# Performance work log

Hardware: AMD Instinct MI355X
Metric: run time of the kernel (lower is better)

Reference implementation:

```python
import jax, jax.numpy as jnp
import numpy as np

B, T, H, A = 64, 512, 1024, 256  # T == max_sen_len by construction of attention_u
PAD_VAL = -2.0 ** 22


def setup_inputs() -> dict:
    key = jax.random.key(0)
    k1, k2, k3, k4 = jax.random.split(key, 4)
    inputs = jax.random.normal(k1, (B, T, H), dtype=jnp.float32)
    sen_len = jax.random.randint(k2, (B,), 1, T + 1, dtype=jnp.int32)
    W = jax.random.normal(k3, (H, A), dtype=jnp.float32) * (1.0 / np.sqrt(H))
    b = jnp.zeros((A,), dtype=jnp.float32)
    U = jax.random.normal(k4, (A, T), dtype=jnp.float32) * (1.0 / np.sqrt(A))
    return {"inputs": inputs, "sen_len": sen_len, "W": W, "b": b, "U": U}


def reference(inputs, sen_len, W, b, U):
    # Dense with tanh: [B,T,H] @ [H,A] -> [B,T,A]
    alpha = jnp.tanh(jnp.einsum('bth,ha->bta', inputs, W) + b)
    # Score against attention_u: [B,T,A] @ [A,T] -> [B,T,T]
    scores = jnp.einsum('bta,as->bts', alpha, U)
    # sequence mask over last (key) dim, broadcast over query dim
    mask = jnp.arange(T)[None, :] < sen_len[:, None]        # [B,T]
    scores = jnp.where(mask[:, None, :], scores, jnp.float32(PAD_VAL))
    p = jax.nn.softmax(scores, axis=-1)                     # [B,T,T]
    # Weighted sum pooling: [B,T,T] @ [B,T,H] -> [B,T,H]
    Z = jnp.einsum('bts,bsh->bth', p, inputs)
    # dropout: is_training=False -> identity
    return Z
```

## Files before the change

### kernel.cpp

```cpp
#include <hip/hip_runtime.h>
#include <hip/hip_bf16.h>

typedef short short8 __attribute__((ext_vector_type(8)));
typedef short short4v __attribute__((ext_vector_type(4)));
typedef float f32x4 __attribute__((ext_vector_type(4)));
typedef __bf16 bf16x8 __attribute__((ext_vector_type(8)));


template <int ROWS>
__device__ __forceinline__ void stage2(const __hip_bfloat16* __restrict__ g,
                                       int ld, short* lds, int t) {
    const int w = t >> 6;
    const int lane = t & 63;
#pragma unroll
    for (int i = 0; i < ROWS / 64; ++i) {
        const int cb = i * 512 + w * 64;
        const int c = cb + lane;
        const int row = c >> 3;
        const int kc = (c & 7) ^ (row & 7);
        __builtin_amdgcn_global_load_lds((const void*)(g + (long)row * ld + kc * 8),
                                         (void*)(lds + cb * 8), 16, 0, 0);
    }
}

template <int BMt, int BNt, int WR, int WC, int ACT_TANH, int STORE_BF16>
__global__ __launch_bounds__(512, 2) void gemm_bt2_kernel(
    const __hip_bfloat16* __restrict__ A, long sA, int lda,
    const __hip_bfloat16* __restrict__ Bt, long sB, int ldb,
    void* __restrict__ Cptr, long sC, int ldc,
    const float* __restrict__ bias, int K) {
    constexpr int MR = BMt / (WR * 16);
    constexpr int NR = BNt / (WC * 16);
    __shared__ __align__(16) short sm[2][(BMt + BNt) * 64];

    int bx = blockIdx.x, by = blockIdx.y, bz = blockIdx.z;
    {
        const int nx = gridDim.x, ny = gridDim.y;
        const int nwg = nx * ny * gridDim.z;
        const int lin = bx + nx * (by + ny * bz);
        const int swz = (lin & 7) * (nwg >> 3) + (lin >> 3);
        bx = swz % nx;
        const int r = swz / nx;
        by = r % ny;
        bz = r / ny;
    }

    const int t = threadIdx.x;
    const int w = t >> 6, lane = t & 63;
    const int wm = w / WC, wn = w % WC;
    const int fr = lane & 15, quad = lane >> 4;

    const __hip_bfloat16* Ab = A + bz * sA + (long)by * BMt * lda;
    const __hip_bfloat16* Bb = Bt + bz * sB + (long)bx * BNt * ldb;

    f32x4 acc[MR][NR] = {};

    const int nk = K / 64;
    stage2<BMt>(Ab, lda, &sm[0][0], t);
    stage2<BNt>(Bb, ldb, &sm[0][BMt * 64], t);
    __syncthreads();

    int cur = 0;
    for (int kt = 0; kt < nk; ++kt) {
        if (kt + 1 < nk) {
            stage2<BMt>(Ab + (kt + 1) * 64, lda, &sm[cur ^ 1][0], t);
            stage2<BNt>(Bb + (kt + 1) * 64, ldb, &sm[cur ^ 1][BMt * 64], t);
        }
        const short* At = &sm[cur][0];
        const short* Bts = &sm[cur][BMt * 64];
#pragma unroll
        for (int ks = 0; ks < 2; ++ks) {
            bf16x8 af[MR], bfv[NR];
            const int kc = ks * 4 + quad;
#pragma unroll
            for (int m = 0; m < MR; ++m) {
                const int row = wm * (MR * 16) + m * 16 + fr;
                const int chunk = row * 8 + (kc ^ (row & 7));
                af[m] = *(const bf16x8*)(const void*)(At + chunk * 8);
            }
#pragma unroll
            for (int n = 0; n < NR; ++n) {
                const int row = wn * (NR * 16) + n * 16 + fr;
                const int chunk = row * 8 + (kc ^ (row & 7));
                bfv[n] = *(const bf16x8*)(const void*)(Bts + chunk * 8);
            }
#pragma unroll
            for (int m = 0; m < MR; ++m)
#pragma unroll
                for (int n = 0; n < NR; ++n)
                    acc[m][n] = __builtin_amdgcn_mfma_f32_16x16x32_bf16(
                        af[m], bfv[n], acc[m][n], 0, 0, 0);
        }
        if (kt + 1 < nk) __syncthreads();
        cur ^= 1;
    }

    const long rowBase = (long)by * BMt + wm * (MR * 16);
    const int colBase = bx * BNt + wn * (NR * 16);
#pragma unroll
    for (int m = 0; m < MR; ++m) {
#pragma unroll
        for (int n = 0; n < NR; ++n) {
            const int col = colBase + n * 16 + fr;
            const float bv = ACT_TANH ? bias[col] : 0.f;
#pragma unroll
            for (int j = 0; j < 4; ++j) {
                const long row = rowBase + m * 16 + quad * 4 + j;
                float v = acc[m][n][j];
                if (ACT_TANH) v = tanhf(v + bv);
                if (STORE_BF16)
                    ((__hip_bfloat16*)Cptr)[bz * sC + row * ldc + col] =
                        __float2bfloat16(v);
                else
                    ((float*)Cptr)[bz * sC + row * ldc + col] = v;
            }
        }
    }
}

__global__ __launch_bounds__(256) void prep_x_kernel(const float* __restrict__ X,
                                                     __hip_bfloat16* __restrict__ Xbf,
                                                     __hip_bfloat16* __restrict__ Xt) {
    __shared__ float tile[64][130];
    const int b = blockIdx.z;
    const int h0 = blockIdx.x * 128, t0 = blockIdx.y * 64;
    const int tid = threadIdx.x;

    const float* Xb = X + ((long)(b * 512 + t0)) * 1024 + h0;
    __hip_bfloat16* Xbfb = Xbf + ((long)(b * 512 + t0)) * 1024 + h0;
#pragma unroll
    for (int p = 0; p < 8; ++p) {
        const int idx = p * 256 + tid;
        const int row = idx >> 5;
        const int c4 = (idx & 31) * 4;
        const float4 v = *(const float4*)(Xb + (long)row * 1024 + c4);
        __hip_bfloat16 tmp[4] __attribute__((aligned(8)));
        tmp[0] = __float2bfloat16(v.x);
        tmp[1] = __float2bfloat16(v.y);
        tmp[2] = __float2bfloat16(v.z);
        tmp[3] = __float2bfloat16(v.w);
        *(short4v*)(void*)(Xbfb + (long)row * 1024 + c4) = *(short4v*)(void*)tmp;
        *(float2*)&tile[row][c4] = make_float2(v.x, v.y);
        *(float2*)&tile[row][c4 + 2] = make_float2(v.z, v.w);
    }
    __syncthreads();

    __hip_bfloat16* Xtb = Xt + ((long)(b * 1024 + h0)) * 512 + t0;
#pragma unroll
    for (int p = 0; p < 4; ++p) {
        const int id = p * 256 + tid;
        const int h = id >> 3;
        const int tc = id & 7;
        __hip_bfloat16 tmp[8] __attribute__((aligned(16)));
#pragma unroll
        for (int j = 0; j < 8; ++j) tmp[j] = __float2bfloat16(tile[8 * tc + j][h]);
        *(short8*)(void*)(Xtb + (long)h * 512 + 8 * tc) = *(short8*)(void*)tmp;
    }
}

__global__ __launch_bounds__(256) void transpose_cvt_kernel(const float* __restrict__ in,
                                                            __hip_bfloat16* __restrict__ out,
                                                            int R, int C) {
    const int o = blockIdx.x * 256 + threadIdx.x;
    if (o >= R * C) return;
    const int c = o / R;
    const int r = o - c * R;
    out[o] = __float2bfloat16(in[(long)r * C + c]);
}

__global__ __launch_bounds__(512) void score_softmax_kernel(
    const __hip_bfloat16* __restrict__ Aa,
    const __hip_bfloat16* __restrict__ Ut,
    __hip_bfloat16* __restrict__ P,
    const int* __restrict__ sen) {
    __shared__ __align__(16) short At[64 * 64];
    __shared__ __align__(16) short Bts[512 * 64];
    __shared__ float red[2][64][9];

    const int t = threadIdx.x;
    const int w = t >> 6, lane = t & 63;
    const int fr = lane & 15, quad = lane >> 4;
    const long row0 = (long)blockIdx.x * 64;
    const __hip_bfloat16* Ab = Aa + row0 * 256;

    f32x4 acc[4][4] = {};

    for (int kt = 0; kt < 4; ++kt) {
        if (kt) __syncthreads();
        {
            const int cb = w * 64;
            const int c = cb + lane;
            const int row = c >> 3, kc = (c & 7) ^ (row & 7);
            __builtin_amdgcn_global_load_lds(
                (const void*)(Ab + (long)row * 256 + kt * 64 + kc * 8),
                (void*)(At + cb * 8), 16, 0, 0);
        }
#pragma unroll
        for (int i = 0; i < 8; ++i) {
            const int cb = i * 512 + w * 64;
            const int c = cb + lane;
            const int row = c >> 3, kc = (c & 7) ^ (row & 7);
            __builtin_amdgcn_global_load_lds(
                (const void*)(Ut + (long)row * 256 + kt * 64 + kc * 8),
                (void*)(Bts + cb * 8), 16, 0, 0);
        }
        __syncthreads();
#pragma unroll
        for (int ks = 0; ks < 2; ++ks) {
            bf16x8 af[4], bfv[4];
            const int kc = ks * 4 + quad;
#pragma unroll
            for (int m = 0; m < 4; ++m) {
                const int row = m * 16 + fr;
                const int chunk = row * 8 + (kc ^ (row & 7));
                af[m] = *(const bf16x8*)(const void*)(At + chunk * 8);
            }
#pragma unroll
            for (int n = 0; n < 4; ++n) {
                const int row = w * 64 + n * 16 + fr;
                const int chunk = row * 8 + (kc ^ (row & 7));
                bfv[n] = *(const bf16x8*)(const void*)(Bts + chunk * 8);
            }
#pragma unroll
            for (int m = 0; m < 4; ++m)
#pragma unroll
                for (int n = 0; n < 4; ++n)
                    acc[m][n] = __builtin_amdgcn_mfma_f32_16x16x32_bf16(
                        af[m], bfv[n], acc[m][n], 0, 0, 0);
        }
    }
    __syncthreads();

    const int L = sen[row0 >> 9];
    bool valid[4];
#pragma unroll
    for (int n = 0; n < 4; ++n) valid[n] = (w * 64 + n * 16 + fr) < L;

    float mx[4][4];
#pragma unroll
    for (int m = 0; m < 4; ++m)
#pragma unroll
        for (int j = 0; j < 4; ++j) {
            float v = -3.0e38f;
#pragma unroll
            for (int n = 0; n < 4; ++n)
                if (valid[n]) v = fmaxf(v, acc[m][n][j]);
#pragma unroll
            for (int off = 8; off >= 1; off >>= 1) v = fmaxf(v, __shfl_xor(v, off, 64));
            mx[m][j] = v;
        }
    if (fr == 0) {
#pragma unroll
        for (int m = 0; m < 4; ++m)
#pragma unroll
            for (int j = 0; j < 4; ++j) red[0][m * 16 + quad * 4 + j][w] = mx[m][j];
    }
    __syncthreads();
    float rmax[4][4];
#pragma unroll
    for (int m = 0; m < 4; ++m)
#pragma unroll
        for (int j = 0; j < 4; ++j) {
            const int row = m * 16 + quad * 4 + j;
            float v = red[0][row][0];
#pragma unroll
            for (int ww = 1; ww < 8; ++ww) v = fmaxf(v, red[0][row][ww]);
            rmax[m][j] = v;
        }

    float sum[4][4];
#pragma unroll
    for (int m = 0; m < 4; ++m)
#pragma unroll
        for (int j = 0; j < 4; ++j) {
            float s = 0.f;
#pragma unroll
            for (int n = 0; n < 4; ++n) {
                float e = valid[n] ? __expf(acc[m][n][j] - rmax[m][j]) : 0.f;
                acc[m][n][j] = e;
                s += e;
            }
#pragma unroll
            for (int off = 8; off >= 1; off >>= 1) s += __shfl_xor(s, off, 64);
            sum[m][j] = s;
        }
    if (fr == 0) {
#pragma unroll
        for (int m = 0; m < 4; ++m)
#pragma unroll
            for (int j = 0; j < 4; ++j) red[1][m * 16 + quad * 4 + j][w] = sum[m][j];
    }
    __syncthreads();
#pragma unroll
    for (int m = 0; m < 4; ++m)
#pragma unroll
        for (int j = 0; j < 4; ++j) {
            const int row = m * 16 + quad * 4 + j;
            float s = 0.f;
#pragma unroll
            for (int ww = 0; ww < 8; ++ww) s += red[1][row][ww];
            const float inv = 1.f / s;
#pragma unroll
            for (int n = 0; n < 4; ++n)
                P[(row0 + row) * 512 + w * 64 + n * 16 + fr] =
                    __float2bfloat16(acc[m][n][j] * inv);
        }
}

extern "C" void kernel_launch(void* const* d_in, const int* in_sizes, int n_in,
                              void* d_out, int out_size, void* d_ws, size_t ws_size,
                              hipStream_t stream) {
    const float* X = (const float*)d_in[0];
    const int* sen = (const int*)d_in[1];
    const float* W = (const float*)d_in[2];
    const float* bias = (const float*)d_in[3];
    const float* U = (const float*)d_in[4];
    float* out = (float*)d_out;

    const int B = 64, T = 512, H = 1024, A = 256;
    const long M = (long)B * T;

    char* ws = (char*)d_ws;
    __hip_bfloat16* Xt = (__hip_bfloat16*)ws;
    __hip_bfloat16* Pbf = (__hip_bfloat16*)(ws + M * H * 2);
    __hip_bfloat16* Wt = (__hip_bfloat16*)(ws + M * H * 2 + M * T * 2);
    __hip_bfloat16* Ut = (__hip_bfloat16*)((char*)Wt + (long)H * A * 2);

    __hip_bfloat16* Xbf = (__hip_bfloat16*)d_out;
    __hip_bfloat16* alpha = (__hip_bfloat16*)((char*)d_out + M * H * 2);

    prep_x_kernel<<<dim3(H / 128, T / 64, B), 256, 0, stream>>>(X, Xbf, Xt);
    transpose_cvt_kernel<<<(H * A) / 256, 256, 0, stream>>>(W, Wt, H, A);
    transpose_cvt_kernel<<<(A * T) / 256, 256, 0, stream>>>(U, Ut, A, T);
    gemm_bt2_kernel<256, 128, 4, 2, 1, 1><<<dim3(A / 128, (int)(M / 256), 1), 512, 0, stream>>>(
        Xbf, 0, H, Wt, 0, H, (void*)alpha, 0, A, bias, H);
    score_softmax_kernel<<<(int)(M / 64), 512, 0, stream>>>(alpha, Ut, Pbf, sen);
    gemm_bt2_kernel<256, 256, 2, 4, 0, 0><<<dim3(H / 256, T / 256, B), 512, 0, stream>>>(
        Pbf, (long)T * T, T, Xt, (long)H * T, T, (void*)out, (long)T * H, H,
        nullptr, T);
}
```

Measured before the change: 165.9 us.

## Fuse fp32-to-bf16 conversion of X into the XW GEMM, drop Xbf buffer

The XW GEMM now reads fp32 X directly, converts it to bf16 in registers and stores it to LDS with a register-prefetch double buffer. This removes the separate bf16 copy of X that prep_x used to write and the GEMM used to read back. The transpose kernel is reworked to tile a full 512-token by 64-hidden block with a swizzled block order. The cost is that both the GEMM and the transpose kernel now read the fp32 X, and the GEMM does its A-tile conversion in the main loop with synchronous global loads.

```diff
diff --git a/kernel.cpp b/kernel.cpp
--- a/kernel.cpp
+++ b/kernel.cpp
@@ -5,7 +5,6 @@
 typedef short short4v __attribute__((ext_vector_type(4)));
 typedef float f32x4 __attribute__((ext_vector_type(4)));
 typedef __bf16 bf16x8 __attribute__((ext_vector_type(8)));
-
 
 template <int ROWS>
 __device__ __forceinline__ void stage2(const __hip_bfloat16* __restrict__ g,
@@ -118,43 +117,170 @@
     }
 }
 
-__global__ __launch_bounds__(256) void prep_x_kernel(const float* __restrict__ X,
-                                                     __hip_bfloat16* __restrict__ Xbf,
-                                                     __hip_bfloat16* __restrict__ Xt) {
-    __shared__ float tile[64][130];
-    const int b = blockIdx.z;
-    const int h0 = blockIdx.x * 128, t0 = blockIdx.y * 64;
+__global__ __launch_bounds__(512) void transpose_x_kernel(
+    const float* __restrict__ X, __hip_bfloat16* __restrict__ Xt) {
+    __shared__ __align__(4) short tile[512 * 66];
+    int bx = blockIdx.x, bz = blockIdx.y;
+    {
+        const int lin = bx + 16 * bz;
+        const int swz = (lin & 7) * 128 + (lin >> 3);
+        bx = swz & 15;
+        bz = swz >> 4;
+    }
     const int tid = threadIdx.x;
-
-    const float* Xb = X + ((long)(b * 512 + t0)) * 1024 + h0;
-    __hip_bfloat16* Xbfb = Xbf + ((long)(b * 512 + t0)) * 1024 + h0;
+    const float* Xb = X + ((long)bz * 512) * 1024 + bx * 64;
+    __hip_bfloat16* ob = Xt + ((long)(bz * 1024 + bx * 64)) * 512;
+
+#pragma unroll
+    for (int p = 0; p < 16; ++p) {
+        const int c = p * 512 + tid;
+        const int t = c >> 4;
+        const int fc = c & 15;
+        const float4 v = *(const float4*)(Xb + (long)t * 1024 + fc * 4);
+        __hip_bfloat16 h0 = __float2bfloat16(v.x), h1 = __float2bfloat16(v.y);
+        __hip_bfloat16 h2 = __float2bfloat16(v.z), h3 = __float2bfloat16(v.w);
+        const int w0 = (int)*(unsigned short*)&h0 | ((int)*(unsigned short*)&h1 << 16);
+        const int w1 = (int)*(unsigned short*)&h2 | ((int)*(unsigned short*)&h3 << 16);
+        int* dst = (int*)(void*)&tile[t * 66 + fc * 4];
+        dst[0] = w0;
+        dst[1] = w1;
+    }
+    __syncthreads();
+
+    const int h = tid >> 3;
+    const int cklo = tid & 7;
 #pragma unroll
     for (int p = 0; p < 8; ++p) {
-        const int idx = p * 256 + tid;
-        const int row = idx >> 5;
-        const int c4 = (idx & 31) * 4;
-        const float4 v = *(const float4*)(Xb + (long)row * 1024 + c4);
-        __hip_bfloat16 tmp[4] __attribute__((aligned(8)));
-        tmp[0] = __float2bfloat16(v.x);
-        tmp[1] = __float2bfloat16(v.y);
-        tmp[2] = __float2bfloat16(v.z);
-        tmp[3] = __float2bfloat16(v.w);
-        *(short4v*)(void*)(Xbfb + (long)row * 1024 + c4) = *(short4v*)(void*)tmp;
-        *(float2*)&tile[row][c4] = make_float2(v.x, v.y);
-        *(float2*)&tile[row][c4 + 2] = make_float2(v.z, v.w);
-    }
-    __syncthreads();
-
-    __hip_bfloat16* Xtb = Xt + ((long)(b * 1024 + h0)) * 512 + t0;
-#pragma unroll
-    for (int p = 0; p < 4; ++p) {
-        const int id = p * 256 + tid;
-        const int h = id >> 3;
-        const int tc = id & 7;
+        const int ck = p * 8 + cklo;
+        short tmp[8] __attribute__((aligned(16)));
+#pragma unroll
+        for (int j = 0; j < 8; ++j) tmp[j] = tile[(8 * ck + j) * 66 + h];
+        *(short8*)(void*)(ob + (long)h * 512 + ck * 8) = *(short8*)(void*)tmp;
+    }
+}
+
+__global__ __launch_bounds__(512, 2) void gemm_xw_kernel(
+    const float* __restrict__ Xf,
+    const __hip_bfloat16* __restrict__ Wt,
+    __hip_bfloat16* __restrict__ alpha,
+    const float* __restrict__ bias) {
+    __shared__ __align__(16) short sm[2][24576];
+
+    int bx = blockIdx.x, by = blockIdx.y;
+    {
+        const int nx = gridDim.x, ny = gridDim.y;
+        const int nwg = nx * ny;
+        const int lin = bx + nx * by;
+        const int swz = (lin & 7) * (nwg >> 3) + (lin >> 3);
+        bx = swz % nx;
+        by = swz / nx;
+    }
+
+    const int t = threadIdx.x;
+    const int w = t >> 6, lane = t & 63;
+    const int wm = w >> 1, wn = w & 1;
+    const int fr = lane & 15, quad = lane >> 4;
+
+    const float* Ab = Xf + (long)by * 256 * 1024;
+    const __hip_bfloat16* Bb = Wt + (long)bx * 128 * 1024;
+
+    int arow[4], akc[4];
+#pragma unroll
+    for (int i = 0; i < 4; ++i) {
+        const int c = i * 512 + t;
+        arow[i] = c >> 3;
+        akc[i] = ((c & 7) ^ (arow[i] & 7)) * 8;
+    }
+
+    f32x4 acc[4][4] = {};
+    float4 rA[4][2];
+
+#pragma unroll
+    for (int i = 0; i < 4; ++i) {
+        const float* src = Ab + (long)arow[i] * 1024 + akc[i];
+        rA[i][0] = *(const float4*)(src);
+        rA[i][1] = *(const float4*)(src + 4);
+    }
+    stage2<128>(Bb, 1024, &sm[0][16384], t);
+#pragma unroll
+    for (int i = 0; i < 4; ++i) {
+        const int c = i * 512 + t;
         __hip_bfloat16 tmp[8] __attribute__((aligned(16)));
-#pragma unroll
-        for (int j = 0; j < 8; ++j) tmp[j] = __float2bfloat16(tile[8 * tc + j][h]);
-        *(short8*)(void*)(Xtb + (long)h * 512 + 8 * tc) = *(short8*)(void*)tmp;
+        tmp[0] = __float2bfloat16(rA[i][0].x); tmp[1] = __float2bfloat16(rA[i][0].y);
+        tmp[2] = __float2bfloat16(rA[i][0].z); tmp[3] = __float2bfloat16(rA[i][0].w);
+        tmp[4] = __float2bfloat16(rA[i][1].x); tmp[5] = __float2bfloat16(rA[i][1].y);
+        tmp[6] = __float2bfloat16(rA[i][1].z); tmp[7] = __float2bfloat16(rA[i][1].w);
+        *(short8*)(void*)&sm[0][c * 8] = *(short8*)(void*)tmp;
+    }
+    __syncthreads();
+
+    int cur = 0;
+    for (int kt = 0; kt < 16; ++kt) {
+        const bool more = kt + 1 < 16;
+        if (more) {
+#pragma unroll
+            for (int i = 0; i < 4; ++i) {
+                const float* src = Ab + (long)arow[i] * 1024 + (kt + 1) * 64 + akc[i];
+                rA[i][0] = *(const float4*)(src);
+                rA[i][1] = *(const float4*)(src + 4);
+            }
+            stage2<128>(Bb + (kt + 1) * 64, 1024, &sm[cur ^ 1][16384], t);
+        }
+        const short* At = &sm[cur][0];
+        const short* Bts = &sm[cur][16384];
+#pragma unroll
+        for (int ks = 0; ks < 2; ++ks) {
+            bf16x8 af[4], bfv[4];
+            const int kc = ks * 4 + quad;
+#pragma unroll
+            for (int m = 0; m < 4; ++m) {
+                const int row = wm * 64 + m * 16 + fr;
+                const int chunk = row * 8 + (kc ^ (row & 7));
+                af[m] = *(const bf16x8*)(const void*)(At + chunk * 8);
+            }
+#pragma unroll
+            for (int n = 0; n < 4; ++n) {
+                const int row = wn * 64 + n * 16 + fr;
+                const int chunk = row * 8 + (kc ^ (row & 7));
+                bfv[n] = *(const bf16x8*)(const void*)(Bts + chunk * 8);
+            }
+#pragma unroll
+            for (int m = 0; m < 4; ++m)
+#pragma unroll
+                for (int n = 0; n < 4; ++n)
+                    acc[m][n] = __builtin_amdgcn_mfma_f32_16x16x32_bf16(
+                        af[m], bfv[n], acc[m][n], 0, 0, 0);
+        }
+        if (more) {
+#pragma unroll
+            for (int i = 0; i < 4; ++i) {
+                const int c = i * 512 + t;
+                __hip_bfloat16 tmp[8] __attribute__((aligned(16)));
+                tmp[0] = __float2bfloat16(rA[i][0].x); tmp[1] = __float2bfloat16(rA[i][0].y);
+                tmp[2] = __float2bfloat16(rA[i][0].z); tmp[3] = __float2bfloat16(rA[i][0].w);
+                tmp[4] = __float2bfloat16(rA[i][1].x); tmp[5] = __float2bfloat16(rA[i][1].y);
+                tmp[6] = __float2bfloat16(rA[i][1].z); tmp[7] = __float2bfloat16(rA[i][1].w);
+                *(short8*)(void*)&sm[cur ^ 1][c * 8] = *(short8*)(void*)tmp;
+            }
+            __syncthreads();
+        }
+        cur ^= 1;
+    }
+
+    const long rowBase = (long)by * 256 + wm * 64;
+    const int colBase = bx * 128 + wn * 64;
+#pragma unroll
+    for (int m = 0; m < 4; ++m) {
+#pragma unroll
+        for (int n = 0; n < 4; ++n) {
+            const int col = colBase + n * 16 + fr;
+            const float bv = bias[col];
+#pragma unroll
+            for (int j = 0; j < 4; ++j) {
+                const long row = rowBase + m * 16 + quad * 4 + j;
+                alpha[row * 256 + col] = __float2bfloat16(tanhf(acc[m][n][j] + bv));
+            }
+        }
     }
 }
 
@@ -326,14 +452,12 @@
     __hip_bfloat16* Wt = (__hip_bfloat16*)(ws + M * H * 2 + M * T * 2);
     __hip_bfloat16* Ut = (__hip_bfloat16*)((char*)Wt + (long)H * A * 2);
 
-    __hip_bfloat16* Xbf = (__hip_bfloat16*)d_out;
     __hip_bfloat16* alpha = (__hip_bfloat16*)((char*)d_out + M * H * 2);
 
-    prep_x_kernel<<<dim3(H / 128, T / 64, B), 256, 0, stream>>>(X, Xbf, Xt);
+    transpose_x_kernel<<<dim3(16, 64), 512, 0, stream>>>(X, Xt);
     transpose_cvt_kernel<<<(H * A) / 256, 256, 0, stream>>>(W, Wt, H, A);
     transpose_cvt_kernel<<<(A * T) / 256, 256, 0, stream>>>(U, Ut, A, T);
-    gemm_bt2_kernel<256, 128, 4, 2, 1, 1><<<dim3(A / 128, (int)(M / 256), 1), 512, 0, stream>>>(
-        Xbf, 0, H, Wt, 0, H, (void*)alpha, 0, A, bias, H);
+    gemm_xw_kernel<<<dim3(2, 128), 512, 0, stream>>>(X, Wt, alpha, bias);
     score_softmax_kernel<<<(int)(M / 64), 512, 0, stream>>>(alpha, Ut, Pbf, sen);
     gemm_bt2_kernel<256, 256, 2, 4, 0, 0><<<dim3(H / 256, T / 256, B), 512, 0, stream>>>(
         Pbf, (long)T * T, T, Xt, (long)H * T, T, (void*)out, (long)T * H, H,
```

After: 174.5 us. +5.2%, slower.
